# Optimization experiments

Measured on AMD Instinct MI355X. Metric: run time of the kernel, lower is better.

The kernel has to match this reference:

```python
import jax, jax.numpy as jnp
import numpy as np

MOS = 100        # max_output_size
IOU_T = 0.9      # iou_threshold
SCORE_T = 0.9    # score_threshold (sigma=0 -> hard NMS; also subsumes the 0.5 decode threshold)
PRE_NMS = 2048   # top-k candidates kept before greedy NMS (fixed-shape jit-friendly form)


def setup_inputs() -> dict:
    key = jax.random.key(0)
    k1, k2 = jax.random.split(key)
    B, H, W, K = 32, 192, 192, 9
    score_map = jax.random.uniform(k1, (B, H, W, K), dtype=jnp.float32)
    delta_map = jax.random.normal(k2, (B, H, W, 4 * K), dtype=jnp.float32) * 0.1
    # realistic normalized grid anchors: 3 scales x 3 aspect ratios, format (xmin, xmax, ymin, ymax)
    scales = jnp.array([0.05, 0.1, 0.2], jnp.float32)
    ratios = jnp.array([0.5, 1.0, 2.0], jnp.float32)
    ws = (scales[:, None] * jnp.sqrt(ratios)[None, :]).reshape(-1)  # [K]
    hs = (scales[:, None] / jnp.sqrt(ratios)[None, :]).reshape(-1)  # [K]
    cx = ((jnp.arange(W, dtype=jnp.float32) + 0.5) / W)[None, :, None]  # [1,W,1]
    cy = ((jnp.arange(H, dtype=jnp.float32) + 0.5) / H)[:, None, None]  # [H,1,1]
    xmin, xmax, ymin, ymax = jnp.broadcast_arrays(cx - ws / 2, cx + ws / 2, cy - hs / 2, cy + hs / 2)
    anchors = jnp.stack([xmin, xmax, ymin, ymax], axis=-1).astype(jnp.float32)  # [H,W,K,4]
    return {"score_map": score_map, "delta_map": delta_map, "anchors": anchors}


def _decode(anchors, deltas):
    # anchors: [H,W,K,4] (xmin,xmax,ymin,ymax); deltas: [B,H,W,K,4] (tx,ty,tw,th)
    xa = (anchors[..., 0] + anchors[..., 1]) * 0.5
    ya = (anchors[..., 2] + anchors[..., 3]) * 0.5
    wa = anchors[..., 1] - anchors[..., 0]
    ha = anchors[..., 3] - anchors[..., 2]
    tx, ty, tw, th = deltas[..., 0], deltas[..., 1], deltas[..., 2], deltas[..., 3]
    x = tx * wa + xa
    y = ty * ha + ya
    w = jnp.exp(tw) * wa
    h = jnp.exp(th) * ha
    # one-sided clips exactly as in the original
    xmin = jnp.maximum(x - w * 0.5, 0.0)
    xmax = jnp.minimum(x + w * 0.5, 1.0)
    ymin = jnp.maximum(y - h * 0.5, 0.0)
    ymax = jnp.minimum(y + h * 0.5, 1.0)
    # original reorders boxes for tf NMS as (ymax, xmin, ymin, xmax) and returns them in that order
    return jnp.stack([ymax, xmin, ymin, xmax], axis=-1)


def _iou_one_vs_all(box, boxes):
    # box layout: (ymax, xmin, ymin, xmax)
    y2a, x1a, y1a, x2a = box[0], box[1], box[2], box[3]
    y2b, x1b, y1b, x2b = boxes[:, 0], boxes[:, 1], boxes[:, 2], boxes[:, 3]
    area_a = jnp.maximum(y2a - y1a, 0.0) * jnp.maximum(x2a - x1a, 0.0)
    area_b = jnp.maximum(y2b - y1b, 0.0) * jnp.maximum(x2b - x1b, 0.0)
    ih = jnp.maximum(jnp.minimum(y2a, y2b) - jnp.maximum(y1a, y1b), 0.0)
    iw = jnp.maximum(jnp.minimum(x2a, x2b) - jnp.maximum(x1a, x1b), 0.0)
    inter = ih * iw
    return inter / (area_a + area_b - inter + 1e-9)


def _nms_one(scores, boxes):
    # scores: [N], boxes: [N,4]. Hard greedy NMS over top PRE_NMS candidates above SCORE_T.
    masked = jnp.where(scores > SCORE_T, scores, -jnp.inf)
    top_s, top_i = jax.lax.top_k(masked, PRE_NMS)
    top_b = boxes[top_i]  # [PRE_NMS, 4]

    def step(s, _):
        idx = jnp.argmax(s)
        valid = s[idx] > SCORE_T
        box = top_b[idx]
        iou = _iou_one_vs_all(box, top_b)
        s = jnp.where(iou > IOU_T, -jnp.inf, s).at[idx].set(-jnp.inf)
        return s, jnp.where(valid, box, jnp.zeros_like(box))

    _, out = jax.lax.scan(step, top_s, None, length=MOS)
    return out  # [MOS, 4], zero-padded past the last kept box


def reference(score_map, delta_map, anchors):
    B = score_map.shape[0]
    H, W, K = anchors.shape[:3]
    deltas = delta_map.reshape(B, H, W, K, 4)
    boxes = _decode(anchors, deltas).reshape(B, H * W * K, 4)
    scores = score_map.reshape(B, H * W * K)
    return jax.vmap(_nms_one)(scores, boxes)  # [B, MOS, 4]
```

## Files before the change

### kernel.cpp

```cpp
#include <hip/hip_runtime.h>
#include <stdint.h>

#pragma clang fp contract(off)

typedef unsigned long long u64;
typedef unsigned int u32;

#define NH 192
#define NW 192
#define NK 9
#define NPB (NH * NW * NK)
#define PRE_NMS 2048
#define CAP 4096
#define FAST_CAP 512
#define FAST_K 256
#define MOS 100
#define SCORE_T_BITS 0x3F666666u
#define ONE_BITS 0x3F800000u
#define IOU_T 0.9f


__global__ void zero_meta(int* __restrict__ meta, int n) {
    int i = blockIdx.x * blockDim.x + threadIdx.x;
    if (i < n) meta[i] = 0;
}

__global__ void hist_kernel(const uint4* __restrict__ scores, int* __restrict__ hist) {
    __shared__ int lh[256];
    const int t = threadIdx.x;
    lh[t] = 0;
    __syncthreads();
    const int b = blockIdx.y;
    const uint4* sp = scores + (size_t)b * (NPB / 4) + (size_t)blockIdx.x * 1024;
#pragma unroll
    for (int i = 0; i < 4; ++i) {
        uint4 v = sp[t + i * 256];
        if (v.x > SCORE_T_BITS) atomicAdd(&lh[(v.x >> 16) & 0xFF], 1);
        if (v.y > SCORE_T_BITS) atomicAdd(&lh[(v.y >> 16) & 0xFF], 1);
        if (v.z > SCORE_T_BITS) atomicAdd(&lh[(v.z >> 16) & 0xFF], 1);
        if (v.w > SCORE_T_BITS) atomicAdd(&lh[(v.w >> 16) & 0xFF], 1);
    }
    __syncthreads();
    if (lh[t] != 0) atomicAdd(&hist[b * 256 + t], lh[t]);
}

__global__ void thresh_kernel(const int* __restrict__ hist, u32* __restrict__ bound, int B) {
    int b = blockIdx.x * blockDim.x + threadIdx.x;
    if (b < B) {
        int cum = 0, tv = 0;
        for (int v = 255; v >= 0; --v) {
            cum += hist[b * 256 + v];
            if (cum >= PRE_NMS) { tv = v; break; }
        }
        u32 bd = ((u32)(0x3F00 + tv)) << 16;
        if (bd < SCORE_T_BITS + 1) bd = SCORE_T_BITS + 1;
        bound[b] = bd;
    }
}

__global__ void compact_kernel(const uint4* __restrict__ scores,
                               const u32* __restrict__ bound,
                               int* __restrict__ cnt,
                               u64* __restrict__ keys) {
    __shared__ u64 stage[4096];
    __shared__ int lcount, lbase;
    const int t = threadIdx.x;
    if (t == 0) lcount = 0;
    __syncthreads();
    const int b = blockIdx.y;
    const u32 bd = bound[b];
    const int base_i = blockIdx.x * 4096;
    const uint4* sp = scores + (size_t)b * (NPB / 4) + (size_t)blockIdx.x * 1024;
#pragma unroll
    for (int i = 0; i < 4; ++i) {
        uint4 v = sp[t + i * 256];
        int ei = base_i + (t + i * 256) * 4;
        u32 uu[4] = {v.x, v.y, v.z, v.w};
#pragma unroll
        for (int c = 0; c < 4; ++c) {
            if (uu[c] >= bd) {
                int p = atomicAdd(&lcount, 1);
                u32 idx = (u32)(ei + c);
                stage[p] = ((u64)uu[c] << 32) | (u64)(~idx);
            }
        }
    }
    __syncthreads();
    if (t == 0) lbase = atomicAdd(&cnt[b], lcount);
    __syncthreads();
    const int nb = lcount, gb = lbase;
    u64* kb = keys + (size_t)b * CAP;
    for (int i = t; i < nb; i += 256) {
        int gp = gb + i;
        if (gp < CAP) kb[gp] = stage[i];
    }
}

__device__ __forceinline__ float4 decode_box(u64 key, int b,
                                             const float4* __restrict__ anchors4,
                                             const float4* __restrict__ deltas4) {
    u32 idx = ~(u32)(key & 0xFFFFFFFFu);
    float4 a = anchors4[idx];
    float4 d = deltas4[(size_t)b * NPB + idx];
    float xa = (a.x + a.y) * 0.5f;
    float ya = (a.z + a.w) * 0.5f;
    float wa = a.y - a.x;
    float ha = a.w - a.z;
    float x = d.x * wa + xa;
    float y = d.y * ha + ya;
    float w = expf(d.z) * wa;
    float h = expf(d.w) * ha;
    float4 bx;
    bx.x = fminf(y + h * 0.5f, 1.f);
    bx.y = fmaxf(x - w * 0.5f, 0.f);
    bx.z = fmaxf(y - h * 0.5f, 0.f);
    bx.w = fminf(x + w * 0.5f, 1.f);
    return bx;
}

__device__ __forceinline__ int wave_nms(const float4* __restrict__ boxes, int n,
                                        float4* __restrict__ out4, int lane) {
    float4 pb0 = make_float4(0.f, 0.f, 0.f, 0.f), pb1 = pb0;
    float pa0 = 0.f, pa1 = 0.f;
    int np = 0;
    float4 nxt = boxes[0];
    for (int j = 0; j < n; ++j) {
        float4 cb = nxt;
        nxt = boxes[(j + 1 < n) ? (j + 1) : j];
        float areab = fmaxf(cb.x - cb.z, 0.f) * fmaxf(cb.w - cb.y, 0.f);
        bool sup = false;
        if (lane < np) {
            float ih = fmaxf(fminf(pb0.x, cb.x) - fmaxf(pb0.z, cb.z), 0.f);
            float iw = fmaxf(fminf(pb0.w, cb.w) - fmaxf(pb0.y, cb.y), 0.f);
            float inter = ih * iw;
            sup = inter / (pa0 + areab - inter + 1e-9f) > IOU_T;
        }
        if (lane + 64 < np) {
            float ih = fmaxf(fminf(pb1.x, cb.x) - fmaxf(pb1.z, cb.z), 0.f);
            float iw = fmaxf(fminf(pb1.w, cb.w) - fmaxf(pb1.y, cb.y), 0.f);
            float inter = ih * iw;
            sup = sup || (inter / (pa1 + areab - inter + 1e-9f) > IOU_T);
        }
        if (!__any(sup)) {
            if (lane == (np & 63)) {
                if (np < 64) { pb0 = cb; pa0 = areab; }
                else         { pb1 = cb; pa1 = areab; }
                out4[np] = cb;
            }
            if (++np == MOS) break;
        }
    }
    return np;
}

__global__ __launch_bounds__(256) void sort_nms_kernel(
        const float* __restrict__ deltas, const float* __restrict__ anchors,
        const int* __restrict__ cnt, const u32* __restrict__ bound,
        const u64* __restrict__ keys, float* __restrict__ out) {
    __shared__ __align__(16) u64 key_s[CAP];
    __shared__ __align__(16) float4 boxes[PRE_NMS];
    __shared__ u64 fast_k[FAST_CAP];
    __shared__ int lh[256];
    __shared__ int s_cnt, s_nsel, s_flag, s_cbin, s_sh;

    const int t = threadIdx.x;
    const int b = blockIdx.x;
    const int nc = min(cnt[b], CAP);
    const u64* kb = keys + (size_t)b * CAP;
    const float4* anchors4 = (const float4*)anchors;
    const float4* deltas4  = (const float4*)deltas;
    float4* out4 = (float4*)out + (size_t)b * MOS;

    lh[t] = 0;
    if (t == 0) {
        s_cnt = 0;
        u32 dmax = ONE_BITS - bound[b];
        int bits = 32 - __builtin_clz(dmax);
        s_sh = (bits > 8) ? (bits - 8) : 0;
    }
    __syncthreads();
    const int sh = s_sh;

#pragma unroll
    for (int p = 0; p < CAP / 256; ++p) {
        int i = t + p * 256;
        u64 k = (i < nc) ? kb[i] : 0ULL;
        key_s[i] = k;
        if (i < nc) {
            u32 d = ONE_BITS - (u32)(k >> 32);
            u32 bin = d >> sh;
            if (bin > 255u) bin = 255u;
            atomicAdd(&lh[bin], 1);
        }
    }
    for (int i = t; i < FAST_CAP; i += 256) fast_k[i] = 0ULL;
    __syncthreads();

    if (t == 0) {
        int cum = 0; bool hit = false;
        for (int v = 0; v < 256; ++v) {
            cum += lh[v];
            if (cum >= FAST_K) {
                if (cum > FAST_CAP) { s_nsel = cum - lh[v]; s_cbin = v - 1; }
                else                { s_nsel = cum;         s_cbin = v; }
                hit = true; break;
            }
        }
        if (!hit) { s_nsel = cum; s_cbin = 255; }
    }
    __syncthreads();
    const int cbin = s_cbin;
    const int n_sel = s_nsel;

#pragma unroll
    for (int p = 0; p < CAP / 256; ++p) {
        int i = t + p * 256;
        if (i < nc) {
            u64 k = key_s[i];
            u32 d = ONE_BITS - (u32)(k >> 32);
            u32 bin = d >> sh;
            if (bin > 255u) bin = 255u;
            if ((int)bin <= cbin) fast_k[atomicAdd(&s_cnt, 1)] = k;
        }
    }
    __syncthreads();

    for (int k = 2; k <= FAST_CAP; k <<= 1) {
        for (int j = k >> 1; j > 0; j >>= 1) {
            for (int i = t; i < FAST_CAP; i += 256) {
                int ix = i ^ j;
                if (ix > i) {
                    u64 a = fast_k[i], c = fast_k[ix];
                    bool up = ((i & k) == 0);
                    if (up ? (a < c) : (a > c)) { fast_k[i] = c; fast_k[ix] = a; }
                }
            }
            __syncthreads();
        }
    }

    for (int i = t; i < FAST_CAP; i += 256)
        boxes[i] = (i < n_sel) ? decode_box(fast_k[i], b, anchors4, deltas4)
                               : make_float4(0.f, 0.f, 0.f, 0.f);
    __syncthreads();

    if (t < 64) {
        int np = wave_nms(boxes, n_sel, out4, t);
        bool success = (np == MOS) || (n_sel == nc);
        if (success)
            for (int i = np + t; i < MOS; i += 64)
                out4[i] = make_float4(0.f, 0.f, 0.f, 0.f);
        if (t == 0) s_flag = success ? 1 : 0;
    }
    __syncthreads();
    if (s_flag) return;

    for (int k = 2; k <= CAP; k <<= 1) {
        for (int j = k >> 1; j > 0; j >>= 1) {
            for (int i = t; i < CAP; i += 256) {
                int ix = i ^ j;
                if (ix > i) {
                    u64 a = key_s[i], c = key_s[ix];
                    bool up = ((i & k) == 0);
                    if (up ? (a < c) : (a > c)) { key_s[i] = c; key_s[ix] = a; }
                }
            }
            __syncthreads();
        }
    }
    const int nvalid = min(nc, PRE_NMS);
    for (int i = t; i < PRE_NMS; i += 256)
        boxes[i] = (i < nvalid) ? decode_box(key_s[i], b, anchors4, deltas4)
                                : make_float4(0.f, 0.f, 0.f, 0.f);
    __syncthreads();
    if (t < 64) {
        int np = wave_nms(boxes, nvalid, out4, t);
        for (int i = np + t; i < MOS; i += 64)
            out4[i] = make_float4(0.f, 0.f, 0.f, 0.f);
    }
}

extern "C" void kernel_launch(void* const* d_in, const int* in_sizes, int n_in,
                              void* d_out, int out_size, void* d_ws, size_t ws_size,
                              hipStream_t stream) {
    const float* score_map = (const float*)d_in[0];
    const float* delta_map = (const float*)d_in[1];
    const float* anchors   = (const float*)d_in[2];
    float* out = (float*)d_out;
    const int B = in_sizes[0] / NPB;

    char* ws = (char*)d_ws;
    int* hist  = (int*)ws;
    int* cnt   = (int*)(ws + (size_t)B * 256 * 4);
    u32* bound = (u32*)(ws + (size_t)B * 256 * 4 + (size_t)B * 4);
    u64* keys  = (u64*)(ws + (size_t)B * 256 * 4 + 2 * (size_t)B * 4);

    const int meta_n = B * 256 + B;
    zero_meta<<<(meta_n + 255) / 256, 256, 0, stream>>>(hist, meta_n);
    hist_kernel<<<dim3(NPB / 4096, B), 256, 0, stream>>>((const uint4*)score_map, hist);
    thresh_kernel<<<1, 256, 0, stream>>>(hist, bound, B);
    compact_kernel<<<dim3(NPB / 4096, B), 256, 0, stream>>>((const uint4*)score_map, bound, cnt, keys);
    sort_nms_kernel<<<B, 256, 0, stream>>>(delta_map, anchors, cnt, bound, keys, out);
}
```

Before: 324.0 us.

## Speculatively compact scores above fixed bound in one pass, repair only on miss

Fuses the histogram and compaction passes by speculatively compacting candidates above a fixed high score bound while building the histogram. A fixup kernel accepts the speculative result when the count lies in the usable range, otherwise recomputes the exact bound and a repair pass recompacts that batch. This removes a full second read of the score map in the common case, at the cost of possibly more candidates entering the sort. The greedy NMS loop is also unrolled to test two candidates per iteration, reducing wave-wide vote rounds.

```diff
diff --git a/kernel.cpp b/kernel.cpp
--- a/kernel.cpp
+++ b/kernel.cpp
@@ -16,6 +16,7 @@
 #define FAST_K 256
 #define MOS 100
 #define SCORE_T_BITS 0x3F666666u
+#define SPEC_BITS   0x3F7E0000u
 #define ONE_BITS 0x3F800000u
 #define IOU_T 0.9f
 
@@ -25,49 +26,78 @@
     if (i < n) meta[i] = 0;
 }
 
-__global__ void hist_kernel(const uint4* __restrict__ scores, int* __restrict__ hist) {
+__global__ void spec_compact_kernel(const uint4* __restrict__ scores,
+                                    int* __restrict__ hist,
+                                    int* __restrict__ cnt,
+                                    u64* __restrict__ keys) {
+    __shared__ u64 stage[4096];
     __shared__ int lh[256];
+    __shared__ int lcount, lbase;
     const int t = threadIdx.x;
     lh[t] = 0;
+    if (t == 0) lcount = 0;
     __syncthreads();
     const int b = blockIdx.y;
+    const int base_i = blockIdx.x * 4096;
     const uint4* sp = scores + (size_t)b * (NPB / 4) + (size_t)blockIdx.x * 1024;
 #pragma unroll
     for (int i = 0; i < 4; ++i) {
         uint4 v = sp[t + i * 256];
-        if (v.x > SCORE_T_BITS) atomicAdd(&lh[(v.x >> 16) & 0xFF], 1);
-        if (v.y > SCORE_T_BITS) atomicAdd(&lh[(v.y >> 16) & 0xFF], 1);
-        if (v.z > SCORE_T_BITS) atomicAdd(&lh[(v.z >> 16) & 0xFF], 1);
-        if (v.w > SCORE_T_BITS) atomicAdd(&lh[(v.w >> 16) & 0xFF], 1);
-    }
-    __syncthreads();
+        int ei = base_i + (t + i * 256) * 4;
+        u32 uu[4] = {v.x, v.y, v.z, v.w};
+#pragma unroll
+        for (int c = 0; c < 4; ++c) {
+            u32 u = uu[c];
+            if (u > SCORE_T_BITS) {
+                atomicAdd(&lh[(u >> 16) & 0xFF], 1);
+                if (u >= SPEC_BITS) {
+                    int p = atomicAdd(&lcount, 1);
+                    u32 idx = (u32)(ei + c);
+                    stage[p] = ((u64)u << 32) | (u64)(~idx);
+                }
+            }
+        }
+    }
+    __syncthreads();
+    if (t == 0) lbase = atomicAdd(&cnt[b], lcount);
     if (lh[t] != 0) atomicAdd(&hist[b * 256 + t], lh[t]);
-}
-
-__global__ void thresh_kernel(const int* __restrict__ hist, u32* __restrict__ bound, int B) {
+    __syncthreads();
+    const int nb = lcount, gb = lbase;
+    u64* kb = keys + (size_t)b * CAP;
+    for (int i = t; i < nb; i += 256) {
+        int gp = gb + i;
+        if (gp < CAP) kb[gp] = stage[i];
+    }
+}
+
+__global__ void fixup_kernel(const int* __restrict__ hist, int* __restrict__ cnt,
+                             u32* __restrict__ bound, int* __restrict__ flag, int B) {
     int b = blockIdx.x * blockDim.x + threadIdx.x;
-    if (b < B) {
-        int cum = 0, tv = 0;
-        for (int v = 255; v >= 0; --v) {
-            cum += hist[b * 256 + v];
-            if (cum >= PRE_NMS) { tv = v; break; }
-        }
-        u32 bd = ((u32)(0x3F00 + tv)) << 16;
-        if (bd < SCORE_T_BITS + 1) bd = SCORE_T_BITS + 1;
-        bound[b] = bd;
-    }
-}
-
-__global__ void compact_kernel(const uint4* __restrict__ scores,
-                               const u32* __restrict__ bound,
-                               int* __restrict__ cnt,
-                               u64* __restrict__ keys) {
+    if (b >= B) return;
+    int c = cnt[b];
+    if (c >= PRE_NMS && c <= CAP) { bound[b] = SPEC_BITS; flag[b] = 0; return; }
+    int cum = 0, tv = 0;
+    for (int v = 255; v >= 0; --v) {
+        cum += hist[b * 256 + v];
+        if (cum >= PRE_NMS) { tv = v; break; }
+    }
+    u32 bd = ((u32)(0x3F00 + tv)) << 16;
+    if (bd < SCORE_T_BITS + 1) bd = SCORE_T_BITS + 1;
+    bound[b] = bd; flag[b] = 1; cnt[b] = 0;
+}
+
+__global__ void repair_compact_kernel(const uint4* __restrict__ scores,
+                                      const u32* __restrict__ bound,
+                                      const int* __restrict__ flag,
+                                      int* __restrict__ cnt,
+                                      u64* __restrict__ keys) {
+    const int b = blockIdx.y;
+    if (!flag[b]) return;
     __shared__ u64 stage[4096];
     __shared__ int lcount, lbase;
     const int t = threadIdx.x;
     if (t == 0) lcount = 0;
     __syncthreads();
-    const int b = blockIdx.y;
     const u32 bd = bound[b];
     const int base_i = blockIdx.x * 4096;
     const uint4* sp = scores + (size_t)b * (NPB / 4) + (size_t)blockIdx.x * 1024;
@@ -123,33 +153,58 @@
     float4 pb0 = make_float4(0.f, 0.f, 0.f, 0.f), pb1 = pb0;
     float pa0 = 0.f, pa1 = 0.f;
     int np = 0;
-    float4 nxt = boxes[0];
-    for (int j = 0; j < n; ++j) {
-        float4 cb = nxt;
-        nxt = boxes[(j + 1 < n) ? (j + 1) : j];
-        float areab = fmaxf(cb.x - cb.z, 0.f) * fmaxf(cb.w - cb.y, 0.f);
-        bool sup = false;
+#define ACCEPT(cb, ar) do { \
+        if (lane == (np & 63)) { \
+            if (np < 64) { pb0 = cb; pa0 = ar; } else { pb1 = cb; pa1 = ar; } \
+            out4[np] = cb; } \
+        ++np; } while (0)
+    for (int j = 0; j < n; j += 2) {
+        const bool have1 = (j + 1 < n);
+        float4 c0 = boxes[j];
+        float4 c1 = boxes[have1 ? j + 1 : j];
+        float ar0 = fmaxf(c0.x - c0.z, 0.f) * fmaxf(c0.w - c0.y, 0.f);
+        float ar1 = fmaxf(c1.x - c1.z, 0.f) * fmaxf(c1.w - c1.y, 0.f);
+        bool s0 = false, s1 = false;
         if (lane < np) {
-            float ih = fmaxf(fminf(pb0.x, cb.x) - fmaxf(pb0.z, cb.z), 0.f);
-            float iw = fmaxf(fminf(pb0.w, cb.w) - fmaxf(pb0.y, cb.y), 0.f);
+            float ih = fmaxf(fminf(pb0.x, c0.x) - fmaxf(pb0.z, c0.z), 0.f);
+            float iw = fmaxf(fminf(pb0.w, c0.w) - fmaxf(pb0.y, c0.y), 0.f);
             float inter = ih * iw;
-            sup = inter / (pa0 + areab - inter + 1e-9f) > IOU_T;
+            s0 = inter / (pa0 + ar0 - inter + 1e-9f) > IOU_T;
+            ih = fmaxf(fminf(pb0.x, c1.x) - fmaxf(pb0.z, c1.z), 0.f);
+            iw = fmaxf(fminf(pb0.w, c1.w) - fmaxf(pb0.y, c1.y), 0.f);
+            inter = ih * iw;
+            s1 = inter / (pa0 + ar1 - inter + 1e-9f) > IOU_T;
         }
         if (lane + 64 < np) {
-            float ih = fmaxf(fminf(pb1.x, cb.x) - fmaxf(pb1.z, cb.z), 0.f);
-            float iw = fmaxf(fminf(pb1.w, cb.w) - fmaxf(pb1.y, cb.y), 0.f);
+            float ih = fmaxf(fminf(pb1.x, c0.x) - fmaxf(pb1.z, c0.z), 0.f);
+            float iw = fmaxf(fminf(pb1.w, c0.w) - fmaxf(pb1.y, c0.y), 0.f);
             float inter = ih * iw;
-            sup = sup || (inter / (pa1 + areab - inter + 1e-9f) > IOU_T);
-        }
-        if (!__any(sup)) {
-            if (lane == (np & 63)) {
-                if (np < 64) { pb0 = cb; pa0 = areab; }
-                else         { pb1 = cb; pa1 = areab; }
-                out4[np] = cb;
-            }
-            if (++np == MOS) break;
-        }
-    }
+            s0 = s0 || (inter / (pa1 + ar0 - inter + 1e-9f) > IOU_T);
+            ih = fmaxf(fminf(pb1.x, c1.x) - fmaxf(pb1.z, c1.z), 0.f);
+            iw = fmaxf(fminf(pb1.w, c1.w) - fmaxf(pb1.y, c1.y), 0.f);
+            inter = ih * iw;
+            s1 = s1 || (inter / (pa1 + ar1 - inter + 1e-9f) > IOU_T);
+        }
+        bool acc0 = !__any(s0);
+        bool acc1 = !__any(s1);
+        if (acc0) {
+            ACCEPT(c0, ar0);
+            if (np == MOS) break;
+            if (have1 && acc1) {
+                float ih = fmaxf(fminf(c0.x, c1.x) - fmaxf(c0.z, c1.z), 0.f);
+                float iw = fmaxf(fminf(c0.w, c1.w) - fmaxf(c0.y, c1.y), 0.f);
+                float inter = ih * iw;
+                if (!(inter / (ar0 + ar1 - inter + 1e-9f) > IOU_T)) {
+                    ACCEPT(c1, ar1);
+                    if (np == MOS) break;
+                }
+            }
+        } else if (have1 && acc1) {
+            ACCEPT(c1, ar1);
+            if (np == MOS) break;
+        }
+    }
+#undef ACCEPT
     return np;
 }
 
@@ -290,15 +345,19 @@
     const int B = in_sizes[0] / NPB;
 
     char* ws = (char*)d_ws;
-    int* hist  = (int*)ws;
-    int* cnt   = (int*)(ws + (size_t)B * 256 * 4);
-    u32* bound = (u32*)(ws + (size_t)B * 256 * 4 + (size_t)B * 4);
-    u64* keys  = (u64*)(ws + (size_t)B * 256 * 4 + 2 * (size_t)B * 4);
+    size_t off = 0;
+    int* hist  = (int*)(ws + off); off += (size_t)B * 256 * 4;
+    int* cnt   = (int*)(ws + off); off += (size_t)B * 4;
+    u32* bound = (u32*)(ws + off); off += (size_t)B * 4;
+    int* flag  = (int*)(ws + off); off += (size_t)B * 4;
+    u64* keys  = (u64*)(ws + off);
 
     const int meta_n = B * 256 + B;
     zero_meta<<<(meta_n + 255) / 256, 256, 0, stream>>>(hist, meta_n);
-    hist_kernel<<<dim3(NPB / 4096, B), 256, 0, stream>>>((const uint4*)score_map, hist);
-    thresh_kernel<<<1, 256, 0, stream>>>(hist, bound, B);
-    compact_kernel<<<dim3(NPB / 4096, B), 256, 0, stream>>>((const uint4*)score_map, bound, cnt, keys);
+    spec_compact_kernel<<<dim3(NPB / 4096, B), 256, 0, stream>>>(
+        (const uint4*)score_map, hist, cnt, keys);
+    fixup_kernel<<<1, 64, 0, stream>>>(hist, cnt, bound, flag, B);
+    repair_compact_kernel<<<dim3(NPB / 4096, B), 256, 0, stream>>>(
+        (const uint4*)score_map, bound, flag, cnt, keys);
     sort_nms_kernel<<<B, 256, 0, stream>>>(delta_map, anchors, cnt, bound, keys, out);
 }
```

New measurement: 301.0 us. 1.08x faster.
